# Performance work log

Hardware: AMD Instinct MI355X
Metric: run time of the kernel (lower is better)

Reference implementation:

```python
import jax, jax.numpy as jnp
import numpy as np

EMB = 512
HEADS = 8


def setup_inputs() -> dict:
    key = jax.random.key(0)
    ks = jax.random.split(key, 5)
    B, N, E = 4, 2048, EMB
    x = jax.random.normal(ks[0], (B, N, E), dtype=jnp.float32)
    # Linear weights stored [in, out] so y = x @ W + b (matches torch x @ W.T + b with W.T)
    W_qkv = jax.random.normal(ks[1], (E, 3 * E), dtype=jnp.float32) * (E ** -0.5)
    b_qkv = jax.random.normal(ks[2], (3 * E,), dtype=jnp.float32) * 0.02
    W_proj = jax.random.normal(ks[3], (E, E), dtype=jnp.float32) * (E ** -0.5)
    b_proj = jax.random.normal(ks[4], (E,), dtype=jnp.float32) * 0.02
    return {"x": x, "W_qkv": W_qkv, "b_qkv": b_qkv, "W_proj": W_proj, "b_proj": b_proj}


def reference(x, W_qkv, b_qkv, W_proj, b_proj):
    B, N, E = x.shape
    H = HEADS
    D = E // H
    qkv = x @ W_qkv + b_qkv                      # [B, N, 3E]
    # einops 'b n (h d qkv) -> qkv b h n d': last dim splits as (h, d, 3) -> q/k/v interleaved
    qkv = qkv.reshape(B, N, H, D, 3)
    q = jnp.transpose(qkv[..., 0], (0, 2, 1, 3))  # [B, H, N, D]
    k = jnp.transpose(qkv[..., 1], (0, 2, 1, 3))
    v = jnp.transpose(qkv[..., 2], (0, 2, 1, 3))
    scale = jnp.asarray(E, x.dtype) ** 0.5        # divides by sqrt(emb_size), as in source
    energies = jnp.einsum('bhqd,bhkd->bhqk', q, k) / scale
    attention = jax.nn.softmax(energies, axis=-1)
    out = jnp.einsum('bhqk,bhkd->bhqd', attention, v)
    out = jnp.transpose(out, (0, 2, 1, 3)).reshape(B, N, E)
    return out @ W_proj + b_proj
```

## Files before the change

### kernel.cpp

```cpp
#include <hip/hip_runtime.h>
#include <hip/hip_bf16.h>

typedef __hip_bfloat16 bf16;
typedef __attribute__((ext_vector_type(8))) short short8;
typedef __attribute__((ext_vector_type(4))) float f32x4;
typedef __attribute__((ext_vector_type(16))) float f32x16;

static constexpr float QSCALE = 1.4426950408889634f / 22.627416997969522f;

__device__ __forceinline__ void gload_lds16(const void* g, void* l) {
  __builtin_amdgcn_global_load_lds((const __attribute__((address_space(1))) unsigned*)(g),
                                   (__attribute__((address_space(3))) unsigned*)(l), 16, 0, 0);
}

__device__ __forceinline__ unsigned cvtpk(float a, float b) {
  unsigned r;
  asm("v_cvt_pk_bf16_f32 %0, %1, %2" : "=v"(r) : "v"(a), "v"(b));
  return r;
}

__device__ __forceinline__ void packP(const f32x16& s, short8* pb) {
#pragma unroll
  for (int g = 0; g < 2; ++g) {
    unsigned a0 = cvtpk(s[8 * g + 0], s[8 * g + 1]);
    unsigned a1 = cvtpk(s[8 * g + 2], s[8 * g + 3]);
    unsigned b0 = cvtpk(s[8 * g + 4], s[8 * g + 5]);
    unsigned b1 = cvtpk(s[8 * g + 6], s[8 * g + 7]);
    asm("v_permlane32_swap_b32 %0, %1" : "+v"(a0), "+v"(b0));
    asm("v_permlane32_swap_b32 %0, %1" : "+v"(a1), "+v"(b1));
    union { unsigned u[4]; short8 v; } pu;
    pu.u[0] = a0; pu.u[1] = a1; pu.u[2] = b0; pu.u[3] = b1;
    pb[g] = pu.v;
  }
}

__global__ __launch_bounds__(256) void cvt_x_kernel(const float* __restrict__ x,
                                                    bf16* __restrict__ xb, int n8) {
  for (int i = blockIdx.x * 256 + threadIdx.x; i < n8; i += gridDim.x * 256) {
    const float4* src = (const float4*)(x) + (size_t)i * 2;
    float4 a = src[0], b = src[1];
    union { short8 v; unsigned u[4]; } o;
    o.u[0] = cvtpk(a.x, a.y);
    o.u[1] = cvtpk(a.z, a.w);
    o.u[2] = cvtpk(b.x, b.y);
    o.u[3] = cvtpk(b.z, b.w);
    *(short8*)(xb + (size_t)i * 8) = o.v;
  }
}

__global__ __launch_bounds__(256) void transpose_cvt(const float* __restrict__ W,
                                                     bf16* __restrict__ Wt,
                                                     int Nout, int permute) {
  __shared__ float tile[64][65];
  const int j0 = blockIdx.x * 64, k0 = blockIdx.y * 64;
  const int tx = threadIdx.x & 63, ty = threadIdx.x >> 6;
  for (int r = ty; r < 64; r += 4)
    tile[r][tx] = W[(size_t)(k0 + r) * Nout + j0 + tx];
  __syncthreads();
  for (int r = ty; r < 64; r += 4) {
    int j = j0 + r;
    int jp = j;
    if (permute) {
      int h = j / 192, rr = j % 192, d = rr / 3, s = rr % 3;
      jp = s * 512 + h * 64 + d;
    }
    Wt[(size_t)jp * 512 + k0 + tx] = __float2bfloat16(tile[tx][r]);
  }
}

template <int MODE>
__global__ __launch_bounds__(256) void gemm_bt(const bf16* __restrict__ A,
                                               const bf16* __restrict__ Bt,
                                               const float* __restrict__ bias,
                                               bf16* __restrict__ Qb, bf16* __restrict__ Kb,
                                               bf16* __restrict__ Vt,
                                               float* __restrict__ Cout) {
  __shared__ short Alds[128 * 32];
  __shared__ short Blds[128 * 32];
  const int t = threadIdx.x;
  const int w = t >> 6;
  const int wr = w >> 1, wc = w & 1;
  const int lr = t & 15;
  const int lq = (t >> 4) & 3;
  const int bm = blockIdx.x, bn = blockIdx.y;

  f32x4 acc[4][4];
#pragma unroll
  for (int m = 0; m < 4; ++m)
#pragma unroll
    for (int n = 0; n < 4; ++n)
#pragma unroll
      for (int j = 0; j < 4; ++j) acc[m][n][j] = 0.f;

  for (int kt = 0; kt < 16; ++kt) {
#pragma unroll
    for (int i = 0; i < 2; ++i) {
      const int c = i * 256 + t;
      gload_lds16(A + (size_t)(bm * 128 + (c >> 2)) * 512 + kt * 32 + (c & 3) * 8,
                  &Alds[(i * 256 + w * 64) * 8]);
      gload_lds16(Bt + (size_t)(bn * 128 + (c >> 2)) * 512 + kt * 32 + (c & 3) * 8,
                  &Blds[(i * 256 + w * 64) * 8]);
    }
    __syncthreads();
    short8 af[4], bfr[4];
#pragma unroll
    for (int m = 0; m < 4; ++m)
      af[m] = *(const short8*)&Alds[(wr * 64 + m * 16 + lr) * 32 + lq * 8];
#pragma unroll
    for (int n = 0; n < 4; ++n)
      bfr[n] = *(const short8*)&Blds[(wc * 64 + n * 16 + lr) * 32 + lq * 8];
#pragma unroll
    for (int m = 0; m < 4; ++m)
#pragma unroll
      for (int n = 0; n < 4; ++n)
        acc[m][n] = __builtin_amdgcn_mfma_f32_16x16x32_bf16(af[m], bfr[n], acc[m][n], 0, 0, 0);
    __syncthreads();
  }

#pragma unroll
  for (int m = 0; m < 4; ++m) {
#pragma unroll
    for (int n = 0; n < 4; ++n) {
      const int col = bn * 128 + wc * 64 + n * 16 + lr;
#pragma unroll
      for (int j = 0; j < 4; ++j) {
        const int row = bm * 128 + wr * 64 + m * 16 + lq * 4 + j;
        float v = acc[m][n][j];
        if (MODE == 0) {
          const int s = col >> 9, h = (col >> 6) & 7, d = col & 63;
          v += bias[h * 192 + d * 3 + s];
          const int hd = col & 511;
          if (s == 0)
            Qb[(size_t)row * 512 + hd] = __float2bfloat16(v * QSCALE);
          else if (s == 1)
            Kb[(size_t)row * 512 + hd] = __float2bfloat16(v);
          else
            Vt[((size_t)((row >> 11) * 8 + h) * 64 + d) * 2048 + (row & 2047)] =
                __float2bfloat16(v);
        } else {
          v += bias[col];
          Cout[(size_t)row * 512 + col] = v;
        }
      }
    }
  }
}

__global__ __launch_bounds__(256, 2) void attn_fwd(const bf16* __restrict__ Q,
                                                   const bf16* __restrict__ K,
                                                   const bf16* __restrict__ Vt,
                                                   bf16* __restrict__ O) {
  __shared__ short Klds[2][64 * 64];
  __shared__ short Vlds[2][64 * 64];
  __shared__ float dnm[2][128];
  const int t = threadIdx.x;
  const int w = t >> 6;
  const int qw = w & 1;
  const int kh = w >> 1;
  const int l = t & 63;
  const int lo = l & 31;
  const int hi = l >> 5;
  const int bid = blockIdx.x;
  const int bh = bid & 31, qt = bid >> 5;
  const int b = bh >> 3, h = bh & 7;
  const int qgA = qt * 128 + qw * 64 + lo;

  const bf16* Kb = K + (size_t)b * 2048 * 512 + h * 64;
  const bf16* Vb = Vt + (size_t)bh * 64 * 2048;

  const bf16* qptrA = Q + ((size_t)b * 2048 + qgA) * 512 + h * 64 + hi * 8;
  short8 qfA[4], qfB[4];
#pragma unroll
  for (int kk = 0; kk < 4; ++kk) {
    qfA[kk] = *(const short8*)(qptrA + kk * 16);
    qfB[kk] = *(const short8*)(qptrA + 32 * 512 + kk * 16);
  }

  union { unsigned u[4]; short8 v; } ones;
#pragma unroll
  for (int j = 0; j < 4; ++j) ones.u[j] = 0x3F803F80u;

  f32x16 zv;
#pragma unroll
  for (int r = 0; r < 16; ++r) zv[r] = 0.f;

  f32x16 accA0, accA1, accB0, accB1;
  f32x16 ssumA, ssumB;
#pragma unroll
  for (int r = 0; r < 16; ++r) {
    accA0[r] = 0.f; accA1[r] = 0.f; accB0[r] = 0.f; accB1[r] = 0.f;
    ssumA[r] = 0.f; ssumB[r] = 0.f;
  }

#define STAGE(BUF, KV0)                                                              \
  do {                                                                               \
    _Pragma("unroll") for (int i = 0; i < 2; ++i) {                                  \
      const int c = i * 256 + t, r = c >> 3, g = (c & 7) ^ (r & 7);                  \
      gload_lds16(Kb + (size_t)((KV0) + r) * 512 + g * 8,                            \
                  &Klds[BUF][(i * 256 + w * 64) * 8]);                               \
    }                                                                                \
    _Pragma("unroll") for (int i = 0; i < 2; ++i) {                                  \
      const int c = i * 256 + t, r = c >> 3, g = (c & 7) ^ (r & 7);                  \
      gload_lds16(Vb + (size_t)r * 2048 + (KV0) + g * 8,                             \
                  &Vlds[BUF][(i * 256 + w * 64) * 8]);                               \
    }                                                                                \
  } while (0)

  STAGE(0, 0);
  __syncthreads();

#pragma unroll 2
  for (int it = 0; it < 32; ++it) {
    const int buf = it & 1;
    if (it + 1 < 32) STAGE(buf ^ 1, (it + 1) * 64);

    const char* kl = (const char*)&Klds[buf][0];
    const char* vl = (const char*)&Vlds[buf][0];

    short8 kf[4];
#pragma unroll
    for (int kk = 0; kk < 4; ++kk)
      kf[kk] = *(const short8*)(kl + ((kh * 32 + lo) << 7) +
                                ((((kk << 1) | hi) ^ (lo & 7)) << 4));

    f32x16 sA, sB;
    __builtin_amdgcn_s_setprio(1);
#pragma unroll
    for (int kk = 0; kk < 4; ++kk) {
      sA = __builtin_amdgcn_mfma_f32_32x32x16_bf16(kf[kk], qfA[kk], kk ? sA : zv, 0, 0, 0);
      sB = __builtin_amdgcn_mfma_f32_32x32x16_bf16(kf[kk], qfB[kk], kk ? sB : zv, 0, 0, 0);
    }
    __builtin_amdgcn_s_setprio(0);

    short8 vf[2][2];
#pragma unroll
    for (int dt = 0; dt < 2; ++dt)
#pragma unroll
      for (int j = 0; j < 2; ++j)
        vf[dt][j] = *(const short8*)(vl + ((dt * 32 + lo) << 7) +
                                     (((((kh * 2 + j) << 1) | hi) ^ (lo & 7)) << 4));

#pragma unroll
    for (int r = 0; r < 16; ++r) sA[r] = __builtin_amdgcn_exp2f(sA[r]);
#pragma unroll
    for (int r = 0; r < 16; ++r) sB[r] = __builtin_amdgcn_exp2f(sB[r]);
    short8 pbA[2], pbB[2];
    packP(sA, pbA);
    packP(sB, pbB);

    __builtin_amdgcn_s_setprio(1);
#pragma unroll
    for (int j = 0; j < 2; ++j) {
      accA0 = __builtin_amdgcn_mfma_f32_32x32x16_bf16(vf[0][j], pbA[j], accA0, 0, 0, 0);
      accA1 = __builtin_amdgcn_mfma_f32_32x32x16_bf16(vf[1][j], pbA[j], accA1, 0, 0, 0);
      accB0 = __builtin_amdgcn_mfma_f32_32x32x16_bf16(vf[0][j], pbB[j], accB0, 0, 0, 0);
      accB1 = __builtin_amdgcn_mfma_f32_32x32x16_bf16(vf[1][j], pbB[j], accB1, 0, 0, 0);
      ssumA = __builtin_amdgcn_mfma_f32_32x32x16_bf16(ones.v, pbA[j], ssumA, 0, 0, 0);
      ssumB = __builtin_amdgcn_mfma_f32_32x32x16_bf16(ones.v, pbB[j], ssumB, 0, 0, 0);
    }
    __builtin_amdgcn_s_setprio(0);

    __syncthreads();
  }
#undef STAGE

  float lsA = ssumA[0], lsB = ssumB[0];
  float* base = qw ? (float*)&Vlds[0][0] : (float*)&Klds[0][0];
  if (kh) {
#pragma unroll
    for (int r = 0; r < 16; ++r) {
      base[l * 64 + ((r + l) & 63)] = accA0[r];
      base[l * 64 + ((16 + r + l) & 63)] = accA1[r];
      base[l * 64 + ((32 + r + l) & 63)] = accB0[r];
      base[l * 64 + ((48 + r + l) & 63)] = accB1[r];
    }
    dnm[qw][l] = lsA;
    dnm[qw][64 + l] = lsB;
  }
  __syncthreads();
  if (!kh) {
#pragma unroll
    for (int r = 0; r < 16; ++r) {
      accA0[r] += base[l * 64 + ((r + l) & 63)];
      accA1[r] += base[l * 64 + ((16 + r + l) & 63)];
      accB0[r] += base[l * 64 + ((32 + r + l) & 63)];
      accB1[r] += base[l * 64 + ((48 + r + l) & 63)];
    }
    lsA += dnm[qw][l];
    lsB += dnm[qw][64 + l];
    const float rlA = 1.0f / lsA;
    const float rlB = 1.0f / lsB;
    bf16* opA = O + ((size_t)b * 2048 + qgA) * 512 + h * 64;
    bf16* opB = opA + 32 * 512;
#pragma unroll
    for (int r = 0; r < 16; ++r) {
      const int d = (r & 3) + 8 * (r >> 2) + 4 * hi;
      opA[d] = __float2bfloat16(accA0[r] * rlA);
      opA[32 + d] = __float2bfloat16(accA1[r] * rlA);
      opB[d] = __float2bfloat16(accB0[r] * rlB);
      opB[32 + d] = __float2bfloat16(accB1[r] * rlB);
    }
  }
}

extern "C" void kernel_launch(void* const* d_in, const int* in_sizes, int n_in,
                              void* d_out, int out_size, void* d_ws, size_t ws_size,
                              hipStream_t stream) {
  const float* x = (const float*)d_in[0];
  const float* Wqkv = (const float*)d_in[1];
  const float* bqkv = (const float*)d_in[2];
  const float* Wproj = (const float*)d_in[3];
  const float* bproj = (const float*)d_in[4];
  float* out = (float*)d_out;

  char* ws = (char*)d_ws;
  bf16* xb = (bf16*)ws;
  bf16* Wqkvt = xb + (size_t)8192 * 512;
  bf16* Wprojt = Wqkvt + (size_t)1536 * 512;
  bf16* Qb = Wprojt + (size_t)512 * 512;
  bf16* Kb = Qb + (size_t)8192 * 512;
  bf16* Vt = Kb + (size_t)8192 * 512;
  bf16* Ob = xb;

  cvt_x_kernel<<<2048, 256, 0, stream>>>(x, xb, 8192 * 512 / 8);
  transpose_cvt<<<dim3(24, 8), 256, 0, stream>>>(Wqkv, Wqkvt, 1536, 1);
  transpose_cvt<<<dim3(8, 8), 256, 0, stream>>>(Wproj, Wprojt, 512, 0);
  gemm_bt<0><<<dim3(64, 12), 256, 0, stream>>>(xb, Wqkvt, bqkv, Qb, Kb, Vt, nullptr);
  attn_fwd<<<512, 256, 0, stream>>>(Qb, Kb, Vt, Ob);
  gemm_bt<1><<<dim3(64, 4), 256, 0, stream>>>(Ob, Wprojt, bproj, nullptr, nullptr, nullptr, out);
}
```

Baseline: 103.6 us.

## Split GEMM into QKV/proj kernels with K=64 tiles, XOR-swizzled LDS, smaller proj tiles

Replaces the templated GEMM with two specialized kernels. Both load K-chunks of 64 instead of 32, halving the barrier count, and XOR-swizzle the LDS layout to avoid bank conflicts on fragment reads. The projection GEMM uses 128x64 tiles so it launches 512 blocks instead of 256 for better CU occupancy. Bias loads are hoisted out of the inner loop. The cost is more LDS per block, which may lower occupancy.

```diff
diff --git a/kernel.cpp b/kernel.cpp
--- a/kernel.cpp
+++ b/kernel.cpp
@@ -68,15 +68,14 @@
   }
 }
 
-template <int MODE>
-__global__ __launch_bounds__(256) void gemm_bt(const bf16* __restrict__ A,
-                                               const bf16* __restrict__ Bt,
-                                               const float* __restrict__ bias,
-                                               bf16* __restrict__ Qb, bf16* __restrict__ Kb,
-                                               bf16* __restrict__ Vt,
-                                               float* __restrict__ Cout) {
-  __shared__ short Alds[128 * 32];
-  __shared__ short Blds[128 * 32];
+__global__ __launch_bounds__(256, 3) void gemm_qkv(const bf16* __restrict__ A,
+                                                   const bf16* __restrict__ Bt,
+                                                   const float* __restrict__ bias,
+                                                   bf16* __restrict__ Qb,
+                                                   bf16* __restrict__ Kb,
+                                                   bf16* __restrict__ Vt) {
+  __shared__ short Alds[128 * 64];
+  __shared__ short Blds[128 * 64];
   const int t = threadIdx.x;
   const int w = t >> 6;
   const int wr = w >> 1, wc = w & 1;
@@ -92,28 +91,37 @@
 #pragma unroll
       for (int j = 0; j < 4; ++j) acc[m][n][j] = 0.f;
 
-  for (int kt = 0; kt < 16; ++kt) {
-#pragma unroll
-    for (int i = 0; i < 2; ++i) {
-      const int c = i * 256 + t;
-      gload_lds16(A + (size_t)(bm * 128 + (c >> 2)) * 512 + kt * 32 + (c & 3) * 8,
+  for (int kt = 0; kt < 8; ++kt) {
+#pragma unroll
+    for (int i = 0; i < 4; ++i) {
+      const int c = i * 256 + t, r = c >> 3, g = (c & 7) ^ (r & 7);
+      gload_lds16(A + (size_t)(bm * 128 + r) * 512 + kt * 64 + g * 8,
                   &Alds[(i * 256 + w * 64) * 8]);
-      gload_lds16(Bt + (size_t)(bn * 128 + (c >> 2)) * 512 + kt * 32 + (c & 3) * 8,
+    }
+#pragma unroll
+    for (int i = 0; i < 4; ++i) {
+      const int c = i * 256 + t, r = c >> 3, g = (c & 7) ^ (r & 7);
+      gload_lds16(Bt + (size_t)(bn * 128 + r) * 512 + kt * 64 + g * 8,
                   &Blds[(i * 256 + w * 64) * 8]);
     }
     __syncthreads();
-    short8 af[4], bfr[4];
-#pragma unroll
-    for (int m = 0; m < 4; ++m)
-      af[m] = *(const short8*)&Alds[(wr * 64 + m * 16 + lr) * 32 + lq * 8];
-#pragma unroll
-    for (int n = 0; n < 4; ++n)
-      bfr[n] = *(const short8*)&Blds[(wc * 64 + n * 16 + lr) * 32 + lq * 8];
-#pragma unroll
-    for (int m = 0; m < 4; ++m)
+#pragma unroll
+    for (int kh2 = 0; kh2 < 2; ++kh2) {
+      short8 af[4], bfr[4];
+#pragma unroll
+      for (int m = 0; m < 4; ++m)
+        af[m] = *(const short8*)&Alds[(wr * 64 + m * 16 + lr) * 64 +
+                                      ((((kh2 << 2) | lq) ^ (lr & 7)) << 3)];
 #pragma unroll
       for (int n = 0; n < 4; ++n)
-        acc[m][n] = __builtin_amdgcn_mfma_f32_16x16x32_bf16(af[m], bfr[n], acc[m][n], 0, 0, 0);
+        bfr[n] = *(const short8*)&Blds[(wc * 64 + n * 16 + lr) * 64 +
+                                       ((((kh2 << 2) | lq) ^ (lr & 7)) << 3)];
+#pragma unroll
+      for (int m = 0; m < 4; ++m)
+#pragma unroll
+        for (int n = 0; n < 4; ++n)
+          acc[m][n] = __builtin_amdgcn_mfma_f32_16x16x32_bf16(af[m], bfr[n], acc[m][n], 0, 0, 0);
+    }
     __syncthreads();
   }
 
@@ -122,25 +130,90 @@
 #pragma unroll
     for (int n = 0; n < 4; ++n) {
       const int col = bn * 128 + wc * 64 + n * 16 + lr;
+      const int s = col >> 9, h = (col >> 6) & 7, d = col & 63;
+      const float bv = bias[h * 192 + d * 3 + s];
+      const int hd = col & 511;
 #pragma unroll
       for (int j = 0; j < 4; ++j) {
         const int row = bm * 128 + wr * 64 + m * 16 + lq * 4 + j;
-        float v = acc[m][n][j];
-        if (MODE == 0) {
-          const int s = col >> 9, h = (col >> 6) & 7, d = col & 63;
-          v += bias[h * 192 + d * 3 + s];
-          const int hd = col & 511;
-          if (s == 0)
-            Qb[(size_t)row * 512 + hd] = __float2bfloat16(v * QSCALE);
-          else if (s == 1)
-            Kb[(size_t)row * 512 + hd] = __float2bfloat16(v);
-          else
-            Vt[((size_t)((row >> 11) * 8 + h) * 64 + d) * 2048 + (row & 2047)] =
-                __float2bfloat16(v);
-        } else {
-          v += bias[col];
-          Cout[(size_t)row * 512 + col] = v;
-        }
+        const float v = acc[m][n][j] + bv;
+        if (s == 0)
+          Qb[(size_t)row * 512 + hd] = __float2bfloat16(v * QSCALE);
+        else if (s == 1)
+          Kb[(size_t)row * 512 + hd] = __float2bfloat16(v);
+        else
+          Vt[((size_t)((row >> 11) * 8 + h) * 64 + d) * 2048 + (row & 2047)] =
+              __float2bfloat16(v);
+      }
+    }
+  }
+}
+
+__global__ __launch_bounds__(256, 2) void gemm_proj(const bf16* __restrict__ A,
+                                                    const bf16* __restrict__ Bt,
+                                                    const float* __restrict__ bias,
+                                                    float* __restrict__ Cout) {
+  __shared__ short Alds[128 * 64];
+  __shared__ short Blds[64 * 64];
+  const int t = threadIdx.x;
+  const int w = t >> 6;
+  const int wr = w >> 1, wc = w & 1;
+  const int lr = t & 15;
+  const int lq = (t >> 4) & 3;
+  const int bm = blockIdx.x, bn = blockIdx.y;
+
+  f32x4 acc[4][2];
+#pragma unroll
+  for (int m = 0; m < 4; ++m)
+#pragma unroll
+    for (int n = 0; n < 2; ++n)
+#pragma unroll
+      for (int j = 0; j < 4; ++j) acc[m][n][j] = 0.f;
+
+  for (int kt = 0; kt < 8; ++kt) {
+#pragma unroll
+    for (int i = 0; i < 4; ++i) {
+      const int c = i * 256 + t, r = c >> 3, g = (c & 7) ^ (r & 7);
+      gload_lds16(A + (size_t)(bm * 128 + r) * 512 + kt * 64 + g * 8,
+                  &Alds[(i * 256 + w * 64) * 8]);
+    }
+#pragma unroll
+    for (int i = 0; i < 2; ++i) {
+      const int c = i * 256 + t, r = c >> 3, g = (c & 7) ^ (r & 7);
+      gload_lds16(Bt + (size_t)(bn * 64 + r) * 512 + kt * 64 + g * 8,
+                  &Blds[(i * 256 + w * 64) * 8]);
+    }
+    __syncthreads();
+#pragma unroll
+    for (int kh2 = 0; kh2 < 2; ++kh2) {
+      short8 af[4], bfr[2];
+#pragma unroll
+      for (int m = 0; m < 4; ++m)
+        af[m] = *(const short8*)&Alds[(wr * 64 + m * 16 + lr) * 64 +
+                                      ((((kh2 << 2) | lq) ^ (lr & 7)) << 3)];
+#pragma unroll
+      for (int n = 0; n < 2; ++n)
+        bfr[n] = *(const short8*)&Blds[(wc * 32 + n * 16 + lr) * 64 +
+                                       ((((kh2 << 2) | lq) ^ (lr & 7)) << 3)];
+#pragma unroll
+      for (int m = 0; m < 4; ++m)
+#pragma unroll
+        for (int n = 0; n < 2; ++n)
+          acc[m][n] = __builtin_amdgcn_mfma_f32_16x16x32_bf16(af[m], bfr[n], acc[m][n], 0, 0, 0);
+    }
+    __syncthreads();
+  }
+
+#pragma unroll
+  for (int m = 0; m < 4; ++m) {
+#pragma unroll
+    for (int n = 0; n < 2; ++n) {
+      const int col = bn * 64 + wc * 32 + n * 16 + lr;
+      const float bv = bias[col];
+#pragma unroll
+      for (int j = 0; j < 4; ++j) {
+        const int row = bm * 128 + wr * 64 + m * 16 + lq * 4 + j;
+        Cout[(size_t)row * 512 + col] = acc[m][n][j] + bv;
       }
     }
   }
@@ -325,7 +398,7 @@
   cvt_x_kernel<<<2048, 256, 0, stream>>>(x, xb, 8192 * 512 / 8);
   transpose_cvt<<<dim3(24, 8), 256, 0, stream>>>(Wqkv, Wqkvt, 1536, 1);
   transpose_cvt<<<dim3(8, 8), 256, 0, stream>>>(Wproj, Wprojt, 512, 0);
-  gemm_bt<0><<<dim3(64, 12), 256, 0, stream>>>(xb, Wqkvt, bqkv, Qb, Kb, Vt, nullptr);
+  gemm_qkv<<<dim3(64, 12), 256, 0, stream>>>(xb, Wqkvt, bqkv, Qb, Kb, Vt);
   attn_fwd<<<512, 256, 0, stream>>>(Qb, Kb, Vt, Ob);
-  gemm_bt<1><<<dim3(64, 4), 256, 0, stream>>>(Ob, Wprojt, bproj, nullptr, nullptr, nullptr, out);
-}
+  gemm_proj<<<dim3(64, 8), 256, 0, stream>>>(Ob, Wprojt, bproj, out);
+}
```

New measurement: 101.9 us. About the same (-1.6%).
